# Optimization experiments

Measured on AMD Instinct MI355X. Metric: run time of the kernel, lower is better.

Reference implementation:

```python
import jax, jax.numpy as jnp
import numpy as np

CHANNEL = 256
REDUCTION = 4
GAMMA = 0.5
H_BW = 1.0  # kernel bandwidth h


def setup_inputs() -> dict:
    key = jax.random.key(0)
    k_x, k1, k2, k3, k4 = jax.random.split(key, 5)
    c, r = CHANNEL, CHANNEL // REDUCTION
    x = jax.random.normal(k_x, (32, c, 64, 64), dtype=jnp.float32)
    # fc params, stored as [in, out] for y = x @ W + b (matches nn.Linear math)
    w1 = jax.random.normal(k1, (c, r), dtype=jnp.float32) * (1.0 / np.sqrt(c))
    b1 = jax.random.normal(k2, (r,), dtype=jnp.float32) * 0.01
    w2 = jax.random.normal(k3, (r, c), dtype=jnp.float32) * (1.0 / np.sqrt(r))
    b2 = jax.random.normal(k4, (c,), dtype=jnp.float32) * 0.01
    return {"x": x, "w1": w1, "b1": b1, "w2": w2, "b2": b2}


def reference(x, w1, b1, w2, b2):
    b, c, Hh, Ww = x.shape
    xf = x.reshape(b, c, Hh * Ww)                      # [b, c, n]
    sq = jnp.sum(xf * xf, axis=-1)                     # [b, c]
    gram = jnp.einsum('bcn,bdn->bcd', xf, xf)          # [b, c, c]
    # ||x_i - x_j||^2 = |x_i|^2 + |x_j|^2 - 2 x_i.x_j  (clamped for numerics)
    d2 = jnp.maximum(sq[:, :, None] + sq[:, None, :] - 2.0 * gram, 0.0)
    K = jnp.exp(-0.5 * d2 / (H_BW * H_BW))             # gaussian kernel on dist
    density = jnp.sum(K, axis=-1) / c                  # [b, c]
    hid = jax.nn.relu(density @ w1 + b1)               # [b, c//r]
    attn = jax.nn.sigmoid(hid @ w2 + b2)               # [b, c]
    return x * (attn[:, :, None, None] + GAMMA)
```

## Files before the change

kernel.cpp:

```cpp
#include <hip/hip_runtime.h>
#include <hip/hip_bf16.h>
#include <cstdint>
#include <cstddef>

#define BATCH 32
#define CH    256
#define NSP   4096
#define RED   64
#define GAMMA 0.5f
#define NSPLIT 4
#define KSEG  (NSP / NSPLIT)
#define NKT   (KSEG / 64)
#define GTILE (CH * CH)
#define SLICE_STRIDE ((size_t)BATCH * GTILE)

typedef float f32x4 __attribute__((ext_vector_type(4)));
typedef short short8 __attribute__((ext_vector_type(8)));

static __device__ inline unsigned short bfu(float f) {
  __hip_bfloat16 h = __float2bfloat16(f);
  return __builtin_bit_cast(unsigned short, h);
}

__global__ __launch_bounds__(512, 4)
void gram_sym_kernel(const float* __restrict__ x, float* __restrict__ gpart) {
  const int bx   = blockIdx.x;
  const int xcd  = bx & 7;
  const int slot = bx >> 3;
  const int g_   = xcd * 16 + (slot >> 2);
  const int q    = slot & 3;
  const int b    = g_ >> 2;
  const int s    = g_ & 3;
  const int tid  = threadIdx.x;
  const int lane = tid & 63;
  const int wave = tid >> 6;

  __shared__ unsigned short panel[256 * 64];

  const int rsub = tid >> 4;
  const int c4   = tid & 15;

  const float* base = x + (size_t)b * CH * NSP + (size_t)s * KSEG;

  f32x4 pa[8];
#pragma unroll
  for (int i = 0; i < 8; ++i) {
    int row = i * 32 + rsub;
    pa[i] = *reinterpret_cast<const f32x4*>(base + (size_t)row * NSP + c4 * 4);
  }

  f32x4 acc[2][4];
#pragma unroll
  for (int m = 0; m < 2; ++m)
#pragma unroll
    for (int n = 0; n < 4; ++n)
      acc[m][n] = (f32x4){0.f, 0.f, 0.f, 0.f};

  char* cP = (char*)panel;

  for (int kt = 0; kt < NKT; ++kt) {
    __syncthreads();
#pragma unroll
    for (int i = 0; i < 8; ++i) {
      int row = i * 32 + rsub;
      int byte = row * 128 + c4 * 8;
      byte ^= (row & 7) << 4;
      uint64_t w = (uint64_t)bfu(pa[i][0]) | ((uint64_t)bfu(pa[i][1]) << 16) |
                   ((uint64_t)bfu(pa[i][2]) << 32) | ((uint64_t)bfu(pa[i][3]) << 48);
      *reinterpret_cast<uint64_t*>(cP + byte) = w;
    }
    __syncthreads();

    if (kt + 1 < NKT) {
      const float* kB = base + (kt + 1) * 64;
#pragma unroll
      for (int i = 0; i < 8; ++i) {
        int row = i * 32 + rsub;
        pa[i] = *reinterpret_cast<const f32x4*>(kB + (size_t)row * NSP + c4 * 4);
      }
    }

#pragma unroll
    for (int kh = 0; kh < 2; ++kh) {
      short8 af[2], bf[4];
#pragma unroll
      for (int m = 0; m < 2; ++m) {
        int rowa = wave * 32 + m * 16 + (lane & 15);
        int bytea = rowa * 128 + kh * 64 + ((lane >> 4) * 16);
        bytea ^= (rowa & 7) << 4;
        af[m] = *reinterpret_cast<const short8*>(cP + bytea);
      }
#pragma unroll
      for (int n = 0; n < 4; ++n) {
        int rowb = q * 64 + n * 16 + (lane & 15);
        int byteb = rowb * 128 + kh * 64 + ((lane >> 4) * 16);
        byteb ^= (rowb & 7) << 4;
        bf[n] = *reinterpret_cast<const short8*>(cP + byteb);
      }
#pragma unroll
      for (int m = 0; m < 2; ++m)
#pragma unroll
        for (int n = 0; n < 4; ++n)
          acc[m][n] = __builtin_amdgcn_mfma_f32_16x16x32_bf16(
              af[m], bf[n], acc[m][n], 0, 0, 0);
    }
  }

  float* g = gpart + ((size_t)s * BATCH + b) * GTILE;
#pragma unroll
  for (int m = 0; m < 2; ++m)
#pragma unroll
    for (int n = 0; n < 4; ++n)
#pragma unroll
      for (int r = 0; r < 4; ++r) {
        int row = wave * 32 + m * 16 + ((lane >> 4) * 4 + r);
        int col = q * 64 + n * 16 + (lane & 15);
        g[(size_t)row * CH + col] = acc[m][n][r];
      }
}

__global__ __launch_bounds__(256)
void density_kernel(const float* __restrict__ gpart, float* __restrict__ density) {
  const int blk  = blockIdx.x;
  const int b    = blk >> 3;
  const int rg   = blk & 7;
  const int t    = threadIdx.x;
  const int lane = t & 63;
  const int wave = t >> 6;

  __shared__ float sq[CH];
  {
    size_t off = (size_t)b * GTILE + (size_t)t * (CH + 1);
    float v = 0.f;
#pragma unroll
    for (int s = 0; s < NSPLIT; ++s) v += gpart[off + (size_t)s * SLICE_STRIDE];
    sq[t] = v;
  }
  __syncthreads();

  const float* gb = gpart + (size_t)b * GTILE;
#pragma unroll 1
  for (int rr = 0; rr < 8; ++rr) {
    int r = rg * 32 + wave * 8 + rr;
    float sqr = sq[r];
    size_t off = (size_t)r * CH + lane * 4;
    f32x4 g = (f32x4){0.f, 0.f, 0.f, 0.f};
#pragma unroll
    for (int s = 0; s < NSPLIT; ++s)
      g += *reinterpret_cast<const f32x4*>(gb + off + (size_t)s * SLICE_STRIDE);
    float ssum = 0.f;
#pragma unroll
    for (int k = 0; k < 4; ++k) {
      float d2 = fmaxf(sqr + sq[lane * 4 + k] - 2.f * g[k], 0.f);
      ssum += __expf(-0.5f * d2);
    }
    ssum += __shfl_xor(ssum, 1);
    ssum += __shfl_xor(ssum, 2);
    ssum += __shfl_xor(ssum, 4);
    ssum += __shfl_xor(ssum, 8);
    ssum += __shfl_xor(ssum, 16);
    ssum += __shfl_xor(ssum, 32);
    if (lane == 0) density[b * CH + r] = ssum * (1.0f / CH);
  }
}

__global__ __launch_bounds__(256)
void mlp_kernel(const float* __restrict__ density,
                const float* __restrict__ w1, const float* __restrict__ b1,
                const float* __restrict__ w2, const float* __restrict__ b2,
                float* __restrict__ scale) {
  const int b = blockIdx.x;
  const int t = threadIdx.x;
  __shared__ float dens[CH];
  __shared__ float hid[RED];
  dens[t] = density[b * CH + t];
  __syncthreads();
  if (t < RED) {
    float s = b1[t];
#pragma unroll 4
    for (int c = 0; c < CH; ++c) s += dens[c] * w1[c * RED + t];
    hid[t] = fmaxf(s, 0.f);
  }
  __syncthreads();
  float s = b2[t];
#pragma unroll
  for (int h = 0; h < RED; ++h) s += hid[h] * w2[h * CH + t];
  scale[b * CH + t] = 1.f / (1.f + __expf(-s)) + GAMMA;
}

__global__ __launch_bounds__(256)
void scale_kernel(const f32x4* __restrict__ x, const float* __restrict__ scale,
                  f32x4* __restrict__ out, int n4) {
  const int stride = gridDim.x * blockDim.x;
  for (int i = blockIdx.x * blockDim.x + threadIdx.x; i < n4; i += stride) {
    float s = scale[i >> 10];
    __builtin_nontemporal_store(x[i] * s, &out[i]);
  }
}

extern "C" void kernel_launch(void* const* d_in, const int* in_sizes, int n_in,
                              void* d_out, int out_size, void* d_ws, size_t ws_size,
                              hipStream_t stream) {
  const float* x  = (const float*)d_in[0];
  const float* w1 = (const float*)d_in[1];
  const float* b1 = (const float*)d_in[2];
  const float* w2 = (const float*)d_in[3];
  const float* b2 = (const float*)d_in[4];
  float* out = (float*)d_out;

  float* gpart   = (float*)d_ws;
  float* density = gpart + NSPLIT * SLICE_STRIDE;
  float* scale   = density + BATCH * CH;

  gram_sym_kernel<<<dim3(512), dim3(512), 0, stream>>>(x, gpart);
  density_kernel<<<dim3(BATCH * 8), dim3(256), 0, stream>>>(gpart, density);
  mlp_kernel<<<dim3(BATCH), dim3(256), 0, stream>>>(density, w1, b1, w2, b2, scale);

  const int n4 = BATCH * CH * NSP / 4;
  scale_kernel<<<dim3(4096), dim3(256), 0, stream>>>(
      (const f32x4*)x, scale, (f32x4*)out, n4);
}
```

Before: 107.7 us.

## Double-buffer LDS panels and prefetch two slabs ahead in gram kernel

The gram kernel now uses two LDS panels and two register slabs. It stages the next panel while computing on the current one, which cuts one barrier per k-tile and keeps two global loads in flight. The cost is doubled LDS (64 KB per block) and 32 extra VGPRs for the second slab. Under launch_bounds(512,4) this may reduce occupancy or cause spills.

```diff
diff --git a/kernel.cpp b/kernel.cpp
--- a/kernel.cpp
+++ b/kernel.cpp
@@ -20,6 +20,54 @@
 static __device__ inline unsigned short bfu(float f) {
   __hip_bfloat16 h = __float2bfloat16(f);
   return __builtin_bit_cast(unsigned short, h);
+}
+
+static __device__ __forceinline__ void stage_panel(char* cP, const f32x4* pa,
+                                                   int rsub, int c4) {
+#pragma unroll
+  for (int i = 0; i < 8; ++i) {
+    int row = i * 32 + rsub;
+    int byte = row * 128 + c4 * 8;
+    byte ^= (row & 7) << 4;
+    uint64_t w = (uint64_t)bfu(pa[i][0]) | ((uint64_t)bfu(pa[i][1]) << 16) |
+                 ((uint64_t)bfu(pa[i][2]) << 32) | ((uint64_t)bfu(pa[i][3]) << 48);
+    *reinterpret_cast<uint64_t*>(cP + byte) = w;
+  }
+}
+
+static __device__ __forceinline__ void load_slab(f32x4* pa, const float* base,
+                                                 int rsub, int c4) {
+#pragma unroll
+  for (int i = 0; i < 8; ++i) {
+    int row = i * 32 + rsub;
+    pa[i] = *reinterpret_cast<const f32x4*>(base + (size_t)row * NSP + c4 * 4);
+  }
+}
+
+static __device__ __forceinline__ void compute_panel(const char* cP, f32x4 acc[2][4],
+                                                     int wave, int q, int lane) {
+#pragma unroll
+  for (int kh = 0; kh < 2; ++kh) {
+    short8 af[2];
+#pragma unroll
+    for (int m = 0; m < 2; ++m) {
+      int rowa = wave * 32 + m * 16 + (lane & 15);
+      int bytea = rowa * 128 + kh * 64 + ((lane >> 4) * 16);
+      bytea ^= (rowa & 7) << 4;
+      af[m] = *reinterpret_cast<const short8*>(cP + bytea);
+    }
+#pragma unroll
+    for (int n = 0; n < 4; ++n) {
+      int rowb = q * 64 + n * 16 + (lane & 15);
+      int byteb = rowb * 128 + kh * 64 + ((lane >> 4) * 16);
+      byteb ^= (rowb & 7) << 4;
+      short8 bf = *reinterpret_cast<const short8*>(cP + byteb);
+#pragma unroll
+      for (int m = 0; m < 2; ++m)
+        acc[m][n] = __builtin_amdgcn_mfma_f32_16x16x32_bf16(
+            af[m], bf, acc[m][n], 0, 0, 0);
+    }
+  }
 }
 
 __global__ __launch_bounds__(512, 4)
@@ -35,20 +83,15 @@
   const int lane = tid & 63;
   const int wave = tid >> 6;
 
-  __shared__ unsigned short panel[256 * 64];
+  __shared__ unsigned short lds0[256 * 64];
+  __shared__ unsigned short lds1[256 * 64];
 
   const int rsub = tid >> 4;
   const int c4   = tid & 15;
 
   const float* base = x + (size_t)b * CH * NSP + (size_t)s * KSEG;
 
-  f32x4 pa[8];
-#pragma unroll
-  for (int i = 0; i < 8; ++i) {
-    int row = i * 32 + rsub;
-    pa[i] = *reinterpret_cast<const f32x4*>(base + (size_t)row * NSP + c4 * 4);
-  }
-
+  f32x4 pa0[8], pa1[8];
   f32x4 acc[2][4];
 #pragma unroll
   for (int m = 0; m < 2; ++m)
@@ -56,54 +99,28 @@
     for (int n = 0; n < 4; ++n)
       acc[m][n] = (f32x4){0.f, 0.f, 0.f, 0.f};
 
-  char* cP = (char*)panel;
-
-  for (int kt = 0; kt < NKT; ++kt) {
+  char* cL0 = (char*)lds0;
+  char* cL1 = (char*)lds1;
+
+  load_slab(pa0, base, rsub, c4);
+  load_slab(pa1, base + 64, rsub, c4);
+  stage_panel(cL0, pa0, rsub, c4);
+  load_slab(pa0, base + 2 * 64, rsub, c4);
+  __syncthreads();
+
+#pragma unroll 1
+  for (int kt = 0; kt < NKT; kt += 2) {
+    stage_panel(cL1, pa1, rsub, c4);
+    if (kt + 3 < NKT) load_slab(pa1, base + (kt + 3) * 64, rsub, c4);
+    compute_panel(cL0, acc, wave, q, lane);
     __syncthreads();
-#pragma unroll
-    for (int i = 0; i < 8; ++i) {
-      int row = i * 32 + rsub;
-      int byte = row * 128 + c4 * 8;
-      byte ^= (row & 7) << 4;
-      uint64_t w = (uint64_t)bfu(pa[i][0]) | ((uint64_t)bfu(pa[i][1]) << 16) |
-                   ((uint64_t)bfu(pa[i][2]) << 32) | ((uint64_t)bfu(pa[i][3]) << 48);
-      *reinterpret_cast<uint64_t*>(cP + byte) = w;
-    }
+
+    if (kt + 2 < NKT) {
+      stage_panel(cL0, pa0, rsub, c4);
+      if (kt + 4 < NKT) load_slab(pa0, base + (kt + 4) * 64, rsub, c4);
+    }
+    compute_panel(cL1, acc, wave, q, lane);
     __syncthreads();
-
-    if (kt + 1 < NKT) {
-      const float* kB = base + (kt + 1) * 64;
-#pragma unroll
-      for (int i = 0; i < 8; ++i) {
-        int row = i * 32 + rsub;
-        pa[i] = *reinterpret_cast<const f32x4*>(kB + (size_t)row * NSP + c4 * 4);
-      }
-    }
-
-#pragma unroll
-    for (int kh = 0; kh < 2; ++kh) {
-      short8 af[2], bf[4];
-#pragma unroll
-      for (int m = 0; m < 2; ++m) {
-        int rowa = wave * 32 + m * 16 + (lane & 15);
-        int bytea = rowa * 128 + kh * 64 + ((lane >> 4) * 16);
-        bytea ^= (rowa & 7) << 4;
-        af[m] = *reinterpret_cast<const short8*>(cP + bytea);
-      }
-#pragma unroll
-      for (int n = 0; n < 4; ++n) {
-        int rowb = q * 64 + n * 16 + (lane & 15);
-        int byteb = rowb * 128 + kh * 64 + ((lane >> 4) * 16);
-        byteb ^= (rowb & 7) << 4;
-        bf[n] = *reinterpret_cast<const short8*>(cP + byteb);
-      }
-#pragma unroll
-      for (int m = 0; m < 2; ++m)
-#pragma unroll
-        for (int n = 0; n < 4; ++n)
-          acc[m][n] = __builtin_amdgcn_mfma_f32_16x16x32_bf16(
-              af[m], bf[n], acc[m][n], 0, 0, 0);
-    }
   }
 
   float* g = gpart + ((size_t)s * BATCH + b) * GTILE;
```

Result: slower. 127.8 us (+18.6%).

## Stream fp32 tiles into double-buffered LDS via direct global-to-LDS loads

Applied to the files above, without the earlier changes.

The gram kernel now moves fp32 data from global memory straight into two alternating LDS buffers using global_load_lds with a K tile of 32. The bf16 conversion moves from before the LDS store to after the LDS read. The aim is to drop the register staging and the separate convert-and-store pass, and to overlap the next tile's load with the current tile's MFMAs using manual vmcnt waits and barriers. In exchange it uses twice the LDS per tile (fp32, double-buffered), repeats the conversion for every fragment read, and has more loop iterations, each with two barriers.

```diff
diff --git a/kernel.cpp b/kernel.cpp
--- a/kernel.cpp
+++ b/kernel.cpp
@@ -10,7 +10,8 @@
 #define GAMMA 0.5f
 #define NSPLIT 4
 #define KSEG  (NSP / NSPLIT)
-#define NKT   (KSEG / 64)
+#define BK    32
+#define NKT   (KSEG / BK)
 #define GTILE (CH * CH)
 #define SLICE_STRIDE ((size_t)BATCH * GTILE)
 
@@ -20,6 +21,15 @@
 static __device__ inline unsigned short bfu(float f) {
   __hip_bfloat16 h = __float2bfloat16(f);
   return __builtin_bit_cast(unsigned short, h);
+}
+
+static __device__ __forceinline__ short8 pack8(f32x4 lo, f32x4 hi) {
+  short8 r;
+  r[0] = (short)bfu(lo[0]); r[1] = (short)bfu(lo[1]);
+  r[2] = (short)bfu(lo[2]); r[3] = (short)bfu(lo[3]);
+  r[4] = (short)bfu(hi[0]); r[5] = (short)bfu(hi[1]);
+  r[6] = (short)bfu(hi[2]); r[7] = (short)bfu(hi[3]);
+  return r;
 }
 
 __global__ __launch_bounds__(512, 4)
@@ -35,18 +45,24 @@
   const int lane = tid & 63;
   const int wave = tid >> 6;
 
-  __shared__ unsigned short panel[256 * 64];
-
-  const int rsub = tid >> 4;
-  const int c4   = tid & 15;
-
-  const float* base = x + (size_t)b * CH * NSP + (size_t)s * KSEG;
-
-  f32x4 pa[8];
-#pragma unroll
-  for (int i = 0; i < 8; ++i) {
-    int row = i * 32 + rsub;
-    pa[i] = *reinterpret_cast<const f32x4*>(base + (size_t)row * NSP + c4 * 4);
+  __shared__ float lds0[256 * BK];
+  __shared__ float lds1[256 * BK];
+
+  const float* xb = x + (size_t)b * CH * NSP + (size_t)s * KSEG;
+
+  const int srow  = lane >> 3;
+  const int sgran = (lane & 7) ^ srow;
+  const float* src[4];
+#pragma unroll
+  for (int j = 0; j < 4; ++j) {
+    int chan = wave * 32 + j * 8 + srow;
+    src[j] = xb + (size_t)chan * NSP + sgran * 4;
+  }
+  float* lb0[4]; float* lb1[4];
+#pragma unroll
+  for (int j = 0; j < 4; ++j) {
+    lb0[j] = lds0 + (wave * 4 + j) * 256;
+    lb1[j] = lds1 + (wave * 4 + j) * 256;
   }
 
   f32x4 acc[2][4];
@@ -56,54 +72,62 @@
     for (int n = 0; n < 4; ++n)
       acc[m][n] = (f32x4){0.f, 0.f, 0.f, 0.f};
 
-  char* cP = (char*)panel;
-
-  for (int kt = 0; kt < NKT; ++kt) {
-    __syncthreads();
-#pragma unroll
-    for (int i = 0; i < 8; ++i) {
-      int row = i * 32 + rsub;
-      int byte = row * 128 + c4 * 8;
-      byte ^= (row & 7) << 4;
-      uint64_t w = (uint64_t)bfu(pa[i][0]) | ((uint64_t)bfu(pa[i][1]) << 16) |
-                   ((uint64_t)bfu(pa[i][2]) << 32) | ((uint64_t)bfu(pa[i][3]) << 48);
-      *reinterpret_cast<uint64_t*>(cP + byte) = w;
-    }
-    __syncthreads();
-
-    if (kt + 1 < NKT) {
-      const float* kB = base + (kt + 1) * 64;
-#pragma unroll
-      for (int i = 0; i < 8; ++i) {
-        int row = i * 32 + rsub;
-        pa[i] = *reinterpret_cast<const f32x4*>(kB + (size_t)row * NSP + c4 * 4);
+  const int g0byte = ((lane >> 4) * 2) << 4;
+  const int rl     = lane & 15;
+
+#pragma unroll
+  for (int j = 0; j < 4; ++j)
+    __builtin_amdgcn_global_load_lds(
+        (const __attribute__((address_space(1))) unsigned int*)(src[j]),
+        (__attribute__((address_space(3))) unsigned int*)(lb0[j]), 16, 0, 0);
+
+#pragma unroll 1
+  for (int t = 0; t < NKT; ++t) {
+    if (t + 1 < NKT) {
+      const int koff = (t + 1) * BK;
+      if ((t + 1) & 1) {
+#pragma unroll
+        for (int j = 0; j < 4; ++j)
+          __builtin_amdgcn_global_load_lds(
+              (const __attribute__((address_space(1))) unsigned int*)(src[j] + koff),
+              (__attribute__((address_space(3))) unsigned int*)(lb1[j]), 16, 0, 0);
+      } else {
+#pragma unroll
+        for (int j = 0; j < 4; ++j)
+          __builtin_amdgcn_global_load_lds(
+              (const __attribute__((address_space(1))) unsigned int*)(src[j] + koff),
+              (__attribute__((address_space(3))) unsigned int*)(lb0[j]), 16, 0, 0);
       }
-    }
-
-#pragma unroll
-    for (int kh = 0; kh < 2; ++kh) {
-      short8 af[2], bf[4];
-#pragma unroll
-      for (int m = 0; m < 2; ++m) {
-        int rowa = wave * 32 + m * 16 + (lane & 15);
-        int bytea = rowa * 128 + kh * 64 + ((lane >> 4) * 16);
-        bytea ^= (rowa & 7) << 4;
-        af[m] = *reinterpret_cast<const short8*>(cP + bytea);
-      }
-#pragma unroll
-      for (int n = 0; n < 4; ++n) {
-        int rowb = q * 64 + n * 16 + (lane & 15);
-        int byteb = rowb * 128 + kh * 64 + ((lane >> 4) * 16);
-        byteb ^= (rowb & 7) << 4;
-        bf[n] = *reinterpret_cast<const short8*>(cP + byteb);
-      }
+      asm volatile("s_waitcnt vmcnt(4)" ::: "memory");
+    } else {
+      asm volatile("s_waitcnt vmcnt(0)" ::: "memory");
+    }
+    __builtin_amdgcn_sched_barrier(0);
+    __builtin_amdgcn_s_barrier();
+
+    const char* cP = (t & 1) ? (const char*)lds1 : (const char*)lds0;
+    short8 af[2];
+#pragma unroll
+    for (int m = 0; m < 2; ++m) {
+      int rowa = wave * 32 + m * 16 + rl;
+      int b1 = rowa * 128 + (g0byte ^ ((rowa & 7) << 4));
+      f32x4 lo = *reinterpret_cast<const f32x4*>(cP + b1);
+      f32x4 hi = *reinterpret_cast<const f32x4*>(cP + (b1 ^ 16));
+      af[m] = pack8(lo, hi);
+    }
+#pragma unroll
+    for (int n = 0; n < 4; ++n) {
+      int rowb = q * 64 + n * 16 + rl;
+      int b1 = rowb * 128 + (g0byte ^ ((rowb & 7) << 4));
+      f32x4 lo = *reinterpret_cast<const f32x4*>(cP + b1);
+      f32x4 hi = *reinterpret_cast<const f32x4*>(cP + (b1 ^ 16));
+      short8 bf = pack8(lo, hi);
 #pragma unroll
       for (int m = 0; m < 2; ++m)
-#pragma unroll
-        for (int n = 0; n < 4; ++n)
-          acc[m][n] = __builtin_amdgcn_mfma_f32_16x16x32_bf16(
-              af[m], bf[n], acc[m][n], 0, 0, 0);
-    }
+        acc[m][n] = __builtin_amdgcn_mfma_f32_16x16x32_bf16(
+            af[m], bf, acc[m][n], 0, 0, 0);
+    }
+    __builtin_amdgcn_s_barrier();
   }
 
   float* g = gpart + ((size_t)s * BATCH + b) * GTILE;
@@ -114,7 +138,7 @@
 #pragma unroll
       for (int r = 0; r < 4; ++r) {
         int row = wave * 32 + m * 16 + ((lane >> 4) * 4 + r);
-        int col = q * 64 + n * 16 + (lane & 15);
+        int col = q * 64 + n * 16 + rl;
         g[(size_t)row * CH + col] = acc[m][n][r];
       }
 }
```

New measurement: 110.8 us. +2.9%, slower.
